# Kernel optimization log

Measured on AMD Instinct MI355X. Metric: run time of the kernel, lower is better.

## Reference

```python
import jax, jax.numpy as jnp
import numpy as np

N_EMBD = 1024
N_HEAD = 16


def setup_inputs() -> dict:
    key = jax.random.key(0)
    k1, k2, k3 = jax.random.split(key, 3)
    B, T, C = 4, 2048, N_EMBD
    x = jax.random.normal(k1, (B, T, C), dtype=jnp.float32)
    # params (bias=False)
    w_attn = jax.random.normal(k2, (C, 3 * C), dtype=jnp.float32) * (C ** -0.5)
    w_proj = jax.random.normal(k3, (C, C), dtype=jnp.float32) * (C ** -0.5)
    return {"x": x, "w_attn": w_attn, "w_proj": w_proj}


def reference(x, w_attn, w_proj):
    B, T, C = x.shape
    H = N_HEAD
    hs = C // H
    qkv = x @ w_attn  # [B,T,3C]
    q, k, v = jnp.split(qkv, 3, axis=-1)
    # [B,H,T,hs]
    q = q.reshape(B, T, H, hs).transpose(0, 2, 1, 3)
    k = k.reshape(B, T, H, hs).transpose(0, 2, 1, 3)
    v = v.reshape(B, T, H, hs).transpose(0, 2, 1, 3)
    wei = jnp.einsum('bhqd,bhkd->bhqk', q, k) * (hs ** -0.5)
    causal = jnp.tril(jnp.ones((T, T), dtype=bool))
    wei = jnp.where(causal[None, None], wei, -jnp.inf)
    wei = jax.nn.softmax(wei, axis=-1)
    # dropout p=0.0 -> identity
    y = jnp.einsum('bhqk,bhkd->bhqd', wei, v)
    y = y.transpose(0, 2, 1, 3).reshape(B, T, C)
    return y @ w_proj
```

## Files before the change

kernel.cpp:

```cpp
#include <hip/hip_runtime.h>
#include <math.h>
#include <stdint.h>

#define B_BATCH 4
#define T_SEQ   2048
#define C_EMB   1024
#define NH      16
#define HS      64

typedef _Float16 half_t;
typedef __attribute__((ext_vector_type(8))) _Float16 half8;
typedef __attribute__((ext_vector_type(4))) _Float16 half4;
typedef __attribute__((ext_vector_type(2))) __fp16 pk16x2;
typedef __attribute__((ext_vector_type(4))) float f32x4;

static __device__ __forceinline__ f32x4 mfma_k16(half4 a, half4 b, f32x4 c) {
#if __has_builtin(__builtin_amdgcn_mfma_f32_16x16x16f16)
    return __builtin_amdgcn_mfma_f32_16x16x16f16(a, b, c, 0, 0, 0);
#else
    half8 a8 = {a.x, a.y, a.z, a.w, (_Float16)0, (_Float16)0, (_Float16)0, (_Float16)0};
    half8 b8 = {b.x, b.y, b.z, b.w, (_Float16)0, (_Float16)0, (_Float16)0, (_Float16)0};
    return __builtin_amdgcn_mfma_f32_16x16x32_f16(a8, b8, c, 0, 0, 0);
#endif
}

static __device__ __forceinline__ void stage16(const void* g, void* lds_base) {
#if __has_builtin(__builtin_amdgcn_global_load_lds)
    __builtin_amdgcn_global_load_lds(
        (const __attribute__((address_space(1))) void*)g,
        (__attribute__((address_space(3))) void*)lds_base, 16, 0, 0);
#else
    const int lane = threadIdx.x & 63;
    ((uint4*)lds_base)[lane] = *(const uint4*)g;
#endif
}

__global__ __launch_bounds__(256) void prep_kernel(const float* __restrict__ x,
                                                   half_t* __restrict__ xh,
                                                   const float* __restrict__ wa,
                                                   half_t* __restrict__ waT,
                                                   const float* __restrict__ wp,
                                                   half_t* __restrict__ wpT) {
    const int blk = blockIdx.x;
    const int tid = threadIdx.x;

    if (blk < 4096) {
        const int i = blk * 256 + tid;
        const float4 a = *(const float4*)(x + (size_t)i * 8);
        const float4 b = *(const float4*)(x + (size_t)i * 8 + 4);
        const pk16x2 h0 = __builtin_amdgcn_cvt_pkrtz(a.x, a.y);
        const pk16x2 h1 = __builtin_amdgcn_cvt_pkrtz(a.z, a.w);
        const pk16x2 h2 = __builtin_amdgcn_cvt_pkrtz(b.x, b.y);
        const pk16x2 h3 = __builtin_amdgcn_cvt_pkrtz(b.z, b.w);
        half8 o = {(_Float16)h0.x, (_Float16)h0.y, (_Float16)h1.x, (_Float16)h1.y,
                   (_Float16)h2.x, (_Float16)h2.y, (_Float16)h3.x, (_Float16)h3.y};
        *(half8*)(xh + (size_t)i * 8) = o;
        return;
    }

    const float* W;
    half_t* WT;
    int K, N, bb;
    if (blk < 4096 + 768) {
        bb = blk - 4096; W = wa; WT = waT; K = 1024; N = 3072;
    } else {
        bb = blk - 4864; W = wp; WT = wpT; K = 1024; N = 1024;
    }
    const int ntiles = N / 64;
    const int n0 = (bb % ntiles) * 64;
    const int k0 = (bb / ntiles) * 64;

    __shared__ float t[64][65];
    const int r = tid >> 4, c4 = (tid & 15) * 4;
#pragma unroll
    for (int p = 0; p < 4; ++p) {
        const float4 g = *(const float4*)(W + (size_t)(k0 + p * 16 + r) * N + n0 + c4);
        t[p * 16 + r][c4 + 0] = g.x;
        t[p * 16 + r][c4 + 1] = g.y;
        t[p * 16 + r][c4 + 2] = g.z;
        t[p * 16 + r][c4 + 3] = g.w;
    }
    __syncthreads();
#pragma unroll
    for (int p = 0; p < 4; ++p) {
        const int n = p * 16 + r;
        half4 s = {(_Float16)t[c4 + 0][n], (_Float16)t[c4 + 1][n],
                   (_Float16)t[c4 + 2][n], (_Float16)t[c4 + 3][n]};
        *(half4*)(WT + (size_t)(n0 + n) * K + k0 + c4) = s;
    }
}

__global__ __launch_bounds__(256) void gemm_bt_f16(const half_t* __restrict__ A,
                                                   const half_t* __restrict__ Bt,
                                                   half_t* __restrict__ Cout,
                                                   int M, int N, int K) {
    __shared__ __align__(16) half_t SM[2 * 128 * 32];
    half_t* As = SM;
    half_t* Bs = SM + 128 * 32;

    const int tid  = threadIdx.x;
    const int lane = tid & 63;
    const int wid  = tid >> 6;
    const int l16  = lane & 15;
    const int quad = lane >> 4;

    const int m0 = blockIdx.y * 128;
    const int n0 = blockIdx.x * 128;
    const int wm = (wid >> 1) * 64;
    const int wn = (wid & 1) * 64;

    const half_t* gA0 = A  + (size_t)(m0 + wid * 16      + (lane >> 2)) * K + (lane & 3) * 8;
    const half_t* gA1 = A  + (size_t)(m0 + wid * 16 + 64 + (lane >> 2)) * K + (lane & 3) * 8;
    const half_t* gB0 = Bt + (size_t)(n0 + wid * 16      + (lane >> 2)) * K + (lane & 3) * 8;
    const half_t* gB1 = Bt + (size_t)(n0 + wid * 16 + 64 + (lane >> 2)) * K + (lane & 3) * 8;

    half_t* lA0 = As + (size_t)wid * 512;
    half_t* lA1 = As + (size_t)(wid + 4) * 512;
    half_t* lB0 = Bs + (size_t)wid * 512;
    half_t* lB1 = Bs + (size_t)(wid + 4) * 512;

    f32x4 acc[4][4];
#pragma unroll
    for (int i = 0; i < 4; ++i)
#pragma unroll
        for (int j = 0; j < 4; ++j) acc[i][j] = (f32x4){0.f, 0.f, 0.f, 0.f};

    for (int k0 = 0; k0 < K; k0 += 32) {
        __syncthreads();
        stage16(gA0 + k0, lA0);
        stage16(gA1 + k0, lA1);
        stage16(gB0 + k0, lB0);
        stage16(gB1 + k0, lB1);
        __syncthreads();

        half8 fa[4], fb[4];
#pragma unroll
        for (int mt = 0; mt < 4; ++mt)
            fa[mt] = *(const half8*)(As + (wm + mt * 16 + l16) * 32 + quad * 8);
#pragma unroll
        for (int nt = 0; nt < 4; ++nt)
            fb[nt] = *(const half8*)(Bs + (wn + nt * 16 + l16) * 32 + quad * 8);
#pragma unroll
        for (int mt = 0; mt < 4; ++mt)
#pragma unroll
            for (int nt = 0; nt < 4; ++nt)
                acc[mt][nt] = __builtin_amdgcn_mfma_f32_16x16x32_f16(
                    fa[mt], fb[nt], acc[mt][nt], 0, 0, 0);
    }

    __syncthreads();
    float* cw = (float*)SM + wid * 1024;
    const int rrow = lane >> 2;
    const int cseg = (lane & 3) * 16;
#pragma unroll
    for (int mt = 0; mt < 4; ++mt) {
#pragma unroll
        for (int nt = 0; nt < 4; ++nt)
            *(f32x4*)&cw[(nt * 16 + l16) * 16 + quad * 4] = acc[mt][nt];
        half_t tmp[16];
#pragma unroll
        for (int jj = 0; jj < 16; ++jj)
            tmp[jj] = (half_t)cw[(cseg + jj) * 16 + rrow];
        half_t* dst = Cout + (size_t)(m0 + wm + mt * 16 + rrow) * N + n0 + wn + cseg;
        *(half8*)(dst)     = *(const half8*)(tmp);
        *(half8*)(dst + 8) = *(const half8*)(tmp + 8);
    }
}

__global__ __launch_bounds__(256) void gemm_bt_a64(const half_t* __restrict__ A,
                                                   const half_t* __restrict__ Bt,
                                                   float* __restrict__ Cout,
                                                   int M, int N, int K) {
    __shared__ half_t As[64 * 32];
    __shared__ half_t Bs[128 * 32];

    const int tid  = threadIdx.x;
    const int lane = tid & 63;
    const int wid  = tid >> 6;
    const int l16  = lane & 15;
    const int quad = lane >> 4;

    const int m0 = blockIdx.y * 64;
    const int n0 = blockIdx.x * 128;
    const int wm = (wid & 1) * 32;
    const int wn = (wid >> 1) * 64;

    const half_t* gA  = A  + (size_t)(m0 + wid * 16      + (lane >> 2)) * K + (lane & 3) * 8;
    const half_t* gB0 = Bt + (size_t)(n0 + wid * 16      + (lane >> 2)) * K + (lane & 3) * 8;
    const half_t* gB1 = Bt + (size_t)(n0 + wid * 16 + 64 + (lane >> 2)) * K + (lane & 3) * 8;

    half_t* lA  = As + (size_t)wid * 512;
    half_t* lB0 = Bs + (size_t)wid * 512;
    half_t* lB1 = Bs + (size_t)(wid + 4) * 512;

    f32x4 acc[2][4];
#pragma unroll
    for (int i = 0; i < 2; ++i)
#pragma unroll
        for (int j = 0; j < 4; ++j) acc[i][j] = (f32x4){0.f, 0.f, 0.f, 0.f};

    for (int k0 = 0; k0 < K; k0 += 32) {
        __syncthreads();
        stage16(gA + k0, lA);
        stage16(gB0 + k0, lB0);
        stage16(gB1 + k0, lB1);
        __syncthreads();

        half8 fa[2], fb[4];
#pragma unroll
        for (int mt = 0; mt < 2; ++mt)
            fa[mt] = *(const half8*)(As + (wm + mt * 16 + l16) * 32 + quad * 8);
#pragma unroll
        for (int nt = 0; nt < 4; ++nt)
            fb[nt] = *(const half8*)(Bs + (wn + nt * 16 + l16) * 32 + quad * 8);
#pragma unroll
        for (int mt = 0; mt < 2; ++mt)
#pragma unroll
            for (int nt = 0; nt < 4; ++nt)
                acc[mt][nt] = __builtin_amdgcn_mfma_f32_16x16x32_f16(
                    fa[mt], fb[nt], acc[mt][nt], 0, 0, 0);
    }

#pragma unroll
    for (int mt = 0; mt < 2; ++mt)
#pragma unroll
        for (int nt = 0; nt < 4; ++nt)
#pragma unroll
            for (int r = 0; r < 4; ++r) {
                const size_t row = m0 + wm + mt * 16 + quad * 4 + r;
                const size_t col = n0 + wn + nt * 16 + l16;
                Cout[row * N + col] = acc[mt][nt][r];
            }
}

#define KL_STRIDE 72
#define VT_STRIDE 72
#define SCALE_EXP2 0.18033688f

__global__ __launch_bounds__(256, 4) void attn_mfma(const half_t* __restrict__ qkv,
                                                    half_t* __restrict__ y) {
    __shared__ half_t Kl[64 * KL_STRIDE];
    __shared__ half_t Vt[64 * VT_STRIDE];
    __shared__ float Lstat[64];

    const int tid  = threadIdx.x;
    const int wid  = tid >> 6;
    const int lane = tid & 63;
    const int l16  = lane & 15;
    const int quad = lane >> 4;

    const int L = blockIdx.x;
    const int g = L & 63;
    const int s = L >> 6;
    const int h = g & 15;
    const int b = g >> 4;

    const size_t rs = 3 * C_EMB;
    const half_t* qb = qkv + (size_t)b * T_SEQ * rs + h * HS;
    const half_t* kb = qb + C_EMB;
    const half_t* vb = qb + 2 * C_EMB;

    const int srow = tid >> 2;
    const int scol = (tid & 3) * 16;
    const int rp   = tid & 31;
    const int dblk = tid >> 5;

    const int qrel = wid * 16 + l16;

#pragma unroll 1
    for (int j = 0; j < 2; ++j) {
        const int qh = (j == 0) ? (31 - s) : s;
        const int q0 = qh * 64;

        __syncthreads();
        {
            const half_t* src = qb + (size_t)(q0 + srow) * rs + scol;
            half_t* dst = Kl + srow * KL_STRIDE + scol;
            *(half8*)(dst)     = *(const half8*)(src);
            *(half8*)(dst + 8) = *(const half8*)(src + 8);
        }
        __syncthreads();

        half8 aQ[2];
#pragma unroll
        for (int s2 = 0; s2 < 2; ++s2)
            aQ[s2] = *(const half8*)(Kl + (wid * 16 + l16) * KL_STRIDE + s2 * 32 + quad * 8);

        f32x4 O[4];
#pragma unroll
        for (int dt = 0; dt < 4; ++dt) O[dt] = (f32x4){0.f, 0.f, 0.f, 0.f};
        float lw = 0.f;

        for (int kt = 0; kt <= qh; ++kt) {
            const int k0 = kt * 64;
            const bool diag = (kt == qh);
            __syncthreads();

            {
                const half_t* src = kb + (size_t)(k0 + srow) * rs + scol;
                half_t* dst = Kl + srow * KL_STRIDE + scol;
                *(half8*)(dst)     = *(const half8*)(src);
                *(half8*)(dst + 8) = *(const half8*)(src + 8);
            }
            {
                const uint4 va = *(const uint4*)(vb + (size_t)(k0 + 2 * rp) * rs + dblk * 8);
                const uint4 vc = *(const uint4*)(vb + (size_t)(k0 + 2 * rp + 1) * rs + dblk * 8);
                const uint32_t a[4] = {va.x, va.y, va.z, va.w};
                const uint32_t c[4] = {vc.x, vc.y, vc.z, vc.w};
                unsigned short* vts = (unsigned short*)Vt;
#pragma unroll
                for (int u = 0; u < 4; ++u) {
                    const int d0 = dblk * 8 + 2 * u;
                    const uint32_t w0 = (a[u] & 0xffffu) | (c[u] << 16);
                    const uint32_t w1 = (a[u] >> 16) | (c[u] & 0xffff0000u);
                    *(uint32_t*)(vts + (d0 + 0) * VT_STRIDE + 2 * rp) = w0;
                    *(uint32_t*)(vts + (d0 + 1) * VT_STRIDE + 2 * rp) = w1;
                }
            }
            __syncthreads();

#pragma unroll
            for (int mt = 0; mt < 4; ++mt) {
                const half8 aK0 = *(const half8*)(Kl + (mt * 16 + l16) * KL_STRIDE + quad * 8);
                const half8 aK1 = *(const half8*)(Kl + (mt * 16 + l16) * KL_STRIDE + 32 + quad * 8);
                f32x4 sa = (f32x4){0.f, 0.f, 0.f, 0.f};
                sa = __builtin_amdgcn_mfma_f32_16x16x32_f16(aK0, aQ[0], sa, 0, 0, 0);
                sa = __builtin_amdgcn_mfma_f32_16x16x32_f16(aK1, aQ[1], sa, 0, 0, 0);

                const int kbase = mt * 16 + quad * 4;
                float p[4];
#pragma unroll
                for (int r = 0; r < 4; ++r)
                    p[r] = __builtin_amdgcn_exp2f(sa[r] * SCALE_EXP2);
                if (diag) {
#pragma unroll
                    for (int r = 0; r < 4; ++r)
                        if (kbase + r > qrel) p[r] = 0.f;
                }
                lw += (p[0] + p[1]) + (p[2] + p[3]);

                const half4 pa = {(_Float16)p[0], (_Float16)p[1],
                                  (_Float16)p[2], (_Float16)p[3]};
#pragma unroll
                for (int dt = 0; dt < 4; ++dt) {
                    const half4 bV = *(const half4*)(Vt + (dt * 16 + l16) * VT_STRIDE +
                                                     mt * 16 + quad * 4);
                    O[dt] = mfma_k16(pa, bV, O[dt]);
                }
            }
        }

        lw += __shfl_xor(lw, 16);
        lw += __shfl_xor(lw, 32);
        if (quad == 0) Lstat[wid * 16 + l16] = lw;
        __syncthreads();
#pragma unroll
        for (int r = 0; r < 4; ++r) {
            const int rowl = wid * 16 + quad * 4 + r;
            const float inv = 1.f / Lstat[rowl];
#pragma unroll
            for (int dt = 0; dt < 4; ++dt)
                Vt[rowl * VT_STRIDE + dt * 16 + l16] = (half_t)(O[dt][r] * inv);
        }
        __syncthreads();
        {
            half_t* dst = y + ((size_t)b * T_SEQ + q0 + srow) * C_EMB + h * HS + scol;
            const half_t* src = Vt + srow * VT_STRIDE + scol;
            *(half8*)(dst)     = *(const half8*)(src);
            *(half8*)(dst + 8) = *(const half8*)(src + 8);
        }
    }
}

extern "C" void kernel_launch(void* const* d_in, const int* in_sizes, int n_in,
                              void* d_out, int out_size, void* d_ws, size_t ws_size,
                              hipStream_t stream) {
    const float* x      = (const float*)d_in[0];
    const float* w_attn = (const float*)d_in[1];
    const float* w_proj = (const float*)d_in[2];
    float* out = (float*)d_out;

    half_t* xh   = (half_t*)d_ws;
    half_t* waT  = xh   + (size_t)8192 * 1024;
    half_t* wpT  = waT  + (size_t)3072 * 1024;
    half_t* qkvh = wpT  + (size_t)1024 * 1024;
    half_t* yh   = qkvh + (size_t)8192 * 3072;

    prep_kernel<<<5120, 256, 0, stream>>>(x, xh, w_attn, waT, w_proj, wpT);

    gemm_bt_f16<<<dim3(24, 64), 256, 0, stream>>>(xh, waT, qkvh, 8192, 3072, 1024);

    attn_mfma<<<dim3(1024), 256, 0, stream>>>(qkvh, yh);

    gemm_bt_a64<<<dim3(8, 128), 256, 0, stream>>>(yh, wpT, out, 8192, 1024, 1024);
}
```

Before: 285.6 us.

## Replace QKV GEMM with 256x256 tiled, software-pipelined, swizzled-LDS kernel

The QKV projection GEMM moves from 128x128 tiles with BK=32 and 256 threads to 256x256 tiles with BK=64 and 512 threads. The new kernel uses XOR-swizzled LDS layouts, interleaves global-to-LDS staging of the next A and B tiles with MFMA groups, uses s_setprio around MFMA bursts, and remaps block IDs across 8 groups to improve L2 locality. The aim is higher arithmetic intensity per LDS byte and overlap of memory traffic with compute. In exchange it uses a 128 KB LDS buffer and more accumulator registers, which limits occupancy, and it relies on hand-written vmcnt waits being correct.

```diff
diff --git a/kernel.cpp b/kernel.cpp
--- a/kernel.cpp
+++ b/kernel.cpp
@@ -90,13 +90,13 @@
     }
 }
 
-__global__ __launch_bounds__(256) void gemm_bt_f16(const half_t* __restrict__ A,
-                                                   const half_t* __restrict__ Bt,
-                                                   half_t* __restrict__ Cout,
-                                                   int M, int N, int K) {
-    __shared__ __align__(16) half_t SM[2 * 128 * 32];
-    half_t* As = SM;
-    half_t* Bs = SM + 128 * 32;
+#define BK2 64
+
+__global__ __launch_bounds__(512, 2) void gemm256(const half_t* __restrict__ A,
+                                                  const half_t* __restrict__ Bt,
+                                                  half_t* __restrict__ Cout,
+                                                  int M, int N, int K) {
+    __shared__ __align__(16) half_t SM[65536];
 
     const int tid  = threadIdx.x;
     const int lane = tid & 63;
@@ -104,48 +104,156 @@
     const int l16  = lane & 15;
     const int quad = lane >> 4;
 
-    const int m0 = blockIdx.y * 128;
-    const int n0 = blockIdx.x * 128;
-    const int wm = (wid >> 1) * 64;
-    const int wn = (wid & 1) * 64;
-
-    const half_t* gA0 = A  + (size_t)(m0 + wid * 16      + (lane >> 2)) * K + (lane & 3) * 8;
-    const half_t* gA1 = A  + (size_t)(m0 + wid * 16 + 64 + (lane >> 2)) * K + (lane & 3) * 8;
-    const half_t* gB0 = Bt + (size_t)(n0 + wid * 16      + (lane >> 2)) * K + (lane & 3) * 8;
-    const half_t* gB1 = Bt + (size_t)(n0 + wid * 16 + 64 + (lane >> 2)) * K + (lane & 3) * 8;
-
-    half_t* lA0 = As + (size_t)wid * 512;
-    half_t* lA1 = As + (size_t)(wid + 4) * 512;
-    half_t* lB0 = Bs + (size_t)wid * 512;
-    half_t* lB1 = Bs + (size_t)(wid + 4) * 512;
-
-    f32x4 acc[4][4];
-#pragma unroll
-    for (int i = 0; i < 4; ++i)
+    const int nwg = gridDim.x;
+    const int cpx = nwg >> 3;
+    const int bid = (blockIdx.x & 7) * cpx + (blockIdx.x >> 3);
+    const int nbx = N >> 8;
+    const int bx = bid % nbx;
+    const int by = bid / nbx;
+    const size_t m0 = (size_t)by << 8;
+    const size_t n0 = (size_t)bx << 8;
+
+    const int warpM = (wid >> 2) * 128;
+    const int wn    = (wid & 3) * 64;
+    const int NTk   = K >> 6;
+
+    const int srow = tid >> 3;
+    const int scsw = (tid & 7) ^ (srow & 7);
+    const half_t* gAs = A  + (m0 + srow) * (size_t)K + scsw * 8;
+    const half_t* gBs = Bt + (n0 + srow) * (size_t)K + scsw * 8;
+
+    f32x4 acc[8][4];
+#pragma unroll
+    for (int i = 0; i < 8; ++i)
 #pragma unroll
         for (int j = 0; j < 4; ++j) acc[i][j] = (f32x4){0.f, 0.f, 0.f, 0.f};
 
-    for (int k0 = 0; k0 < K; k0 += 32) {
-        __syncthreads();
-        stage16(gA0 + k0, lA0);
-        stage16(gA1 + k0, lA1);
-        stage16(gB0 + k0, lB0);
-        stage16(gB1 + k0, lB1);
-        __syncthreads();
-
-        half8 fa[4], fb[4];
-#pragma unroll
-        for (int mt = 0; mt < 4; ++mt)
-            fa[mt] = *(const half8*)(As + (wm + mt * 16 + l16) * 32 + quad * 8);
-#pragma unroll
-        for (int nt = 0; nt < 4; ++nt)
-            fb[nt] = *(const half8*)(Bs + (wn + nt * 16 + l16) * 32 + quad * 8);
-#pragma unroll
-        for (int mt = 0; mt < 4; ++mt)
-#pragma unroll
-            for (int nt = 0; nt < 4; ++nt)
-                acc[mt][nt] = __builtin_amdgcn_mfma_f32_16x16x32_f16(
-                    fa[mt], fb[nt], acc[mt][nt], 0, 0, 0);
+    auto ldA = [&](const half_t* Ab, int mt, int kk) -> half8 {
+        const int r = warpM + mt * 16 + l16;
+        const int c = (kk * 4 + quad) ^ (l16 & 7);
+        return *(const half8*)(Ab + r * 64 + c * 8);
+    };
+    auto ldB = [&](const half_t* Bb, int nt, int kk) -> half8 {
+        const int r = wn + nt * 16 + l16;
+        const int c = (kk * 4 + quad) ^ (l16 & 7);
+        return *(const half8*)(Bb + r * 64 + c * 8);
+    };
+
+#pragma unroll
+    for (int s = 0; s < 4; ++s)
+        stage16(gAs + (size_t)(s * 64) * K, SM + s * 4096 + wid * 512);
+#pragma unroll
+    for (int s = 0; s < 4; ++s)
+        stage16(gBs + (size_t)(s * 64) * K, SM + 16384 + s * 4096 + wid * 512);
+    if (NTk > 1) {
+#pragma unroll
+        for (int s = 0; s < 4; ++s)
+            stage16(gBs + (size_t)(s * 64) * K + BK2, SM + 49152 + s * 4096 + wid * 512);
+        asm volatile("s_waitcnt vmcnt(4)" ::: "memory");
+    } else {
+        asm volatile("s_waitcnt vmcnt(0)" ::: "memory");
+    }
+    __builtin_amdgcn_s_barrier();
+    __builtin_amdgcn_sched_barrier(0);
+
+    auto tile_body = [&](int t, half_t* Ac, half_t* Bc, half_t* An) {
+        const int kA = (t + 1) * BK2;
+        const int kB = (t + 2) * BK2;
+        const bool doA = (t + 1) < NTk;
+        const bool doB = (t + 2) < NTk;
+
+        half8 fb[4][2];
+
+        if (doA) {
+            stage16(gAs + (size_t)(0 * 64) * K + kA, An + 0 * 4096 + wid * 512);
+            stage16(gAs + (size_t)(1 * 64) * K + kA, An + 1 * 4096 + wid * 512);
+        }
+#pragma unroll
+        for (int nt = 0; nt < 4; ++nt) {
+            fb[nt][0] = ldB(Bc, nt, 0);
+            fb[nt][1] = ldB(Bc, nt, 1);
+        }
+        {
+            half8 a00 = ldA(Ac, 0, 0), a01 = ldA(Ac, 0, 1);
+            half8 a10 = ldA(Ac, 1, 0), a11 = ldA(Ac, 1, 1);
+            __builtin_amdgcn_s_barrier();
+            __builtin_amdgcn_s_setprio(1);
+#pragma unroll
+            for (int nt = 0; nt < 4; ++nt) {
+                acc[0][nt] = __builtin_amdgcn_mfma_f32_16x16x32_f16(a00, fb[nt][0], acc[0][nt], 0, 0, 0);
+                acc[0][nt] = __builtin_amdgcn_mfma_f32_16x16x32_f16(a01, fb[nt][1], acc[0][nt], 0, 0, 0);
+                acc[1][nt] = __builtin_amdgcn_mfma_f32_16x16x32_f16(a10, fb[nt][0], acc[1][nt], 0, 0, 0);
+                acc[1][nt] = __builtin_amdgcn_mfma_f32_16x16x32_f16(a11, fb[nt][1], acc[1][nt], 0, 0, 0);
+            }
+            __builtin_amdgcn_s_setprio(0);
+        }
+        if (doA) {
+            stage16(gAs + (size_t)(2 * 64) * K + kA, An + 2 * 4096 + wid * 512);
+            stage16(gAs + (size_t)(3 * 64) * K + kA, An + 3 * 4096 + wid * 512);
+        }
+        {
+            half8 a00 = ldA(Ac, 2, 0), a01 = ldA(Ac, 2, 1);
+            half8 a10 = ldA(Ac, 3, 0), a11 = ldA(Ac, 3, 1);
+            __builtin_amdgcn_s_barrier();
+            __builtin_amdgcn_s_setprio(1);
+#pragma unroll
+            for (int nt = 0; nt < 4; ++nt) {
+                acc[2][nt] = __builtin_amdgcn_mfma_f32_16x16x32_f16(a00, fb[nt][0], acc[2][nt], 0, 0, 0);
+                acc[2][nt] = __builtin_amdgcn_mfma_f32_16x16x32_f16(a01, fb[nt][1], acc[2][nt], 0, 0, 0);
+                acc[3][nt] = __builtin_amdgcn_mfma_f32_16x16x32_f16(a10, fb[nt][0], acc[3][nt], 0, 0, 0);
+                acc[3][nt] = __builtin_amdgcn_mfma_f32_16x16x32_f16(a11, fb[nt][1], acc[3][nt], 0, 0, 0);
+            }
+            __builtin_amdgcn_s_setprio(0);
+        }
+        if (doB) {
+            stage16(gBs + (size_t)(0 * 64) * K + kB, Bc + 0 * 4096 + wid * 512);
+            stage16(gBs + (size_t)(1 * 64) * K + kB, Bc + 1 * 4096 + wid * 512);
+        }
+        {
+            half8 a00 = ldA(Ac, 4, 0), a01 = ldA(Ac, 4, 1);
+            half8 a10 = ldA(Ac, 5, 0), a11 = ldA(Ac, 5, 1);
+            __builtin_amdgcn_s_barrier();
+            __builtin_amdgcn_s_setprio(1);
+#pragma unroll
+            for (int nt = 0; nt < 4; ++nt) {
+                acc[4][nt] = __builtin_amdgcn_mfma_f32_16x16x32_f16(a00, fb[nt][0], acc[4][nt], 0, 0, 0);
+                acc[4][nt] = __builtin_amdgcn_mfma_f32_16x16x32_f16(a01, fb[nt][1], acc[4][nt], 0, 0, 0);
+                acc[5][nt] = __builtin_amdgcn_mfma_f32_16x16x32_f16(a10, fb[nt][0], acc[5][nt], 0, 0, 0);
+                acc[5][nt] = __builtin_amdgcn_mfma_f32_16x16x32_f16(a11, fb[nt][1], acc[5][nt], 0, 0, 0);
+            }
+            __builtin_amdgcn_s_setprio(0);
+        }
+        if (doB) {
+            stage16(gBs + (size_t)(2 * 64) * K + kB, Bc + 2 * 4096 + wid * 512);
+            stage16(gBs + (size_t)(3 * 64) * K + kB, Bc + 3 * 4096 + wid * 512);
+        }
+        {
+            half8 a00 = ldA(Ac, 6, 0), a01 = ldA(Ac, 6, 1);
+            half8 a10 = ldA(Ac, 7, 0), a11 = ldA(Ac, 7, 1);
+            __builtin_amdgcn_s_barrier();
+            __builtin_amdgcn_s_setprio(1);
+#pragma unroll
+            for (int nt = 0; nt < 4; ++nt) {
+                acc[6][nt] = __builtin_amdgcn_mfma_f32_16x16x32_f16(a00, fb[nt][0], acc[6][nt], 0, 0, 0);
+                acc[6][nt] = __builtin_amdgcn_mfma_f32_16x16x32_f16(a01, fb[nt][1], acc[6][nt], 0, 0, 0);
+                acc[7][nt] = __builtin_amdgcn_mfma_f32_16x16x32_f16(a10, fb[nt][0], acc[7][nt], 0, 0, 0);
+                acc[7][nt] = __builtin_amdgcn_mfma_f32_16x16x32_f16(a11, fb[nt][1], acc[7][nt], 0, 0, 0);
+            }
+            __builtin_amdgcn_s_setprio(0);
+        }
+        if (doB) {
+            asm volatile("s_waitcnt vmcnt(4)" ::: "memory");
+        } else if (doA) {
+            asm volatile("s_waitcnt vmcnt(0)" ::: "memory");
+        }
+        __builtin_amdgcn_s_barrier();
+        __builtin_amdgcn_sched_barrier(0);
+    };
+
+    for (int tt = 0; tt < NTk; tt += 2) {
+        tile_body(tt, SM, SM + 16384, SM + 32768);
+        if (tt + 1 < NTk)
+            tile_body(tt + 1, SM + 32768, SM + 49152, SM);
     }
 
     __syncthreads();
@@ -153,7 +261,7 @@
     const int rrow = lane >> 2;
     const int cseg = (lane & 3) * 16;
 #pragma unroll
-    for (int mt = 0; mt < 4; ++mt) {
+    for (int mt = 0; mt < 8; ++mt) {
 #pragma unroll
         for (int nt = 0; nt < 4; ++nt)
             *(f32x4*)&cw[(nt * 16 + l16) * 16 + quad * 4] = acc[mt][nt];
@@ -161,7 +269,7 @@
 #pragma unroll
         for (int jj = 0; jj < 16; ++jj)
             tmp[jj] = (half_t)cw[(cseg + jj) * 16 + rrow];
-        half_t* dst = Cout + (size_t)(m0 + wm + mt * 16 + rrow) * N + n0 + wn + cseg;
+        half_t* dst = Cout + (m0 + warpM + mt * 16 + rrow) * (size_t)N + n0 + wn + cseg;
         *(half8*)(dst)     = *(const half8*)(tmp);
         *(half8*)(dst + 8) = *(const half8*)(tmp + 8);
     }
@@ -388,7 +496,7 @@
 
     prep_kernel<<<5120, 256, 0, stream>>>(x, xh, w_attn, waT, w_proj, wpT);
 
-    gemm_bt_f16<<<dim3(24, 64), 256, 0, stream>>>(xh, waT, qkvh, 8192, 3072, 1024);
+    gemm256<<<dim3(384), 512, 0, stream>>>(xh, waT, qkvh, 8192, 3072, 1024);
 
     attn_mfma<<<dim3(1024), 256, 0, stream>>>(qkvh, yh);
 
```

Measured after the change: 268.1 us. 6.1% less time.
